# Performance work log

Measured on AMD Instinct MI355X. Metric: run time of the kernel, lower is better.

## Reference

```python
import jax, jax.numpy as jnp
import numpy as np


def _binop(ei, ej):
    # diagonal linear recurrence combine: (a_i, b_i) * (a_j, b_j) -> (a_j*a_i, a_j*b_i + b_j)
    ai, bi = ei
    aj, bj = ej
    return aj * ai, aj * bi + bj


def setup_inputs() -> dict:
    key = jax.random.key(0)
    ks = jax.random.split(key, 9)
    B_, T, D_in, D_out, N = 16, 2048, 512, 512, 512
    inp = {
        "input": jax.random.normal(ks[0], (B_, T, D_in), dtype=jnp.float32),
        "D": jax.random.normal(ks[1], (D_out, D_in), dtype=jnp.float32) / np.sqrt(D_in),
        "nu_log": jax.random.normal(ks[2], (N,), dtype=jnp.float32),
        "theta_log": jax.random.normal(ks[3], (N,), dtype=jnp.float32),
        "gamma_log": jax.random.normal(ks[4], (N,), dtype=jnp.float32),
        "B_re": jax.random.normal(ks[5], (N, D_in), dtype=jnp.float32) / np.sqrt(2 * D_in),
        "B_im": jax.random.normal(ks[6], (N, D_in), dtype=jnp.float32) / np.sqrt(2 * D_in),
        "C_re": jax.random.normal(ks[7], (D_out, N), dtype=jnp.float32) / np.sqrt(N),
        "C_im": jax.random.normal(ks[8], (D_out, N), dtype=jnp.float32) / np.sqrt(N),
    }
    return inp


def reference(input, D, nu_log, theta_log, gamma_log, B_re, B_im, C_re, C_im):
    # ss_params
    lam_abs = jnp.exp(-jnp.exp(nu_log))                      # [N]
    lam_phase = jnp.exp(theta_log)                           # [N]
    lam = lam_abs * (jnp.cos(lam_phase) + 1j * jnp.sin(lam_phase))  # complex [N]
    gamma = jnp.exp(gamma_log)                               # [N]
    Bc = (B_re + 1j * B_im) * gamma[:, None]                 # [N, D_in]
    Cc = C_re + 1j * C_im                                    # [D_out, N]

    # input projection: Bu_elements [batch, T, N] (complex)
    Bu = input.astype(Bc.dtype) @ Bc.T
    lam_el = jnp.broadcast_to(lam, Bu.shape)

    # parallel associative scan over time axis (initial state is zero)
    _, states = jax.lax.associative_scan(_binop, (lam_el, Bu), axis=1)

    # readout
    y = jnp.real(states @ Cc.T) + input @ D.T                # [batch, T, D_out]
    return y
```

## Files before the change

kernel.cpp:

```cpp
#include <hip/hip_runtime.h>
#include <hip/hip_fp16.h>

typedef _Float16 f16;
typedef __attribute__((ext_vector_type(8))) _Float16 f16x8;
typedef __attribute__((ext_vector_type(2))) _Float16 f16x2;
typedef __attribute__((ext_vector_type(4))) float f32x4;

#define B_SZ 16
#define T_SZ 2048
#define DIN 512
#define DOUT 512
#define N_SZ 512
#define M_SZ (B_SZ * T_SZ)
#define NCHUNK 16
#define LCHUNK 128

__device__ __forceinline__ void gload_lds16(const void* g, void* l) {
  __builtin_amdgcn_global_load_lds(
      (const __attribute__((address_space(1))) void*)g,
      (__attribute__((address_space(3))) void*)l, 16, 0, 0);
}


__global__ void prep_params(const float* __restrict__ nu_log,
                            const float* __restrict__ theta_log,
                            float2* __restrict__ lam2,
                            float2* __restrict__ lamL2) {
  int n = threadIdx.x;
  if (n < N_SZ) {
    float nu = expf(nu_log[n]);
    float ph = expf(theta_log[n]);
    float la = expf(-nu);
    lam2[n] = make_float2(la * cosf(ph), la * sinf(ph));
    float laL = expf(-nu * (float)LCHUNK);
    float phL = ph * (float)LCHUNK;
    lamL2[n] = make_float2(laL * cosf(phL), laL * sinf(phL));
  }
}

__global__ void prep_w1(const float* __restrict__ B_re, const float* __restrict__ B_im,
                        const float* __restrict__ gamma_log, f16* __restrict__ W1) {
  int tid = blockIdx.x * 256 + threadIdx.x;
  int np = tid >> 9;
  int d = tid & 511;
  int n = np >> 1;
  float g = expf(gamma_log[n]);
  const float* src = (np & 1) ? B_im : B_re;
  W1[(size_t)np * 512 + d] = (f16)(src[(size_t)n * 512 + d] * g);
}

__global__ void prep_w2(const float* __restrict__ C_re, const float* __restrict__ C_im,
                        const float* __restrict__ Dm, f16* __restrict__ W2) {
  int k = blockIdx.x * 256 + threadIdx.x;
  int j = blockIdx.y;
  float v;
  if (k < 512)       v =  C_re[(size_t)j * 512 + k];
  else if (k < 1024) v = -C_im[(size_t)j * 512 + (k - 512)];
  else               v =  Dm[(size_t)j * 512 + (k - 1024)];
  W2[(size_t)j * 1536 + k] = (f16)v;
}

__global__ void conv_input(const float* __restrict__ in, f16* __restrict__ A2) {
  int tid = blockIdx.x * 256 + threadIdx.x;
  int m = tid >> 6;
  int d0 = (tid & 63) << 3;
  const float4* p = (const float4*)(in + (size_t)m * DIN + d0);
  float4 a = p[0], b = p[1];
  f16x8 h;
  h[0] = (f16)a.x; h[1] = (f16)a.y; h[2] = (f16)a.z; h[3] = (f16)a.w;
  h[4] = (f16)b.x; h[5] = (f16)b.y; h[6] = (f16)b.z; h[7] = (f16)b.w;
  *(f16x8*)(A2 + (size_t)m * 1536 + 1024 + d0) = h;
}


__global__ void scan_a(const f16* __restrict__ Bu, const float2* __restrict__ lam2,
                       float2* __restrict__ S) {
  int tid = blockIdx.x * 256 + threadIdx.x;
  int n = tid & 511;
  int c = (tid >> 9) & (NCHUNK - 1);
  int b = tid >> 13;
  float2 l = lam2[n];
  const unsigned* bu = (const unsigned*)Bu + (size_t)(b * T_SZ + c * LCHUNK) * 512 + n;
  float sre = 0.f, sim = 0.f;
#pragma unroll 8
  for (int t = 0; t < LCHUNK; ++t) {
    unsigned u = bu[(size_t)t * 512];
    f16x2 h = __builtin_bit_cast(f16x2, u);
    float nre = l.x * sre - l.y * sim + (float)h.x;
    sim = l.x * sim + l.y * sre + (float)h.y;
    sre = nre;
  }
  S[(size_t)(b * NCHUNK + c) * 512 + n] = make_float2(sre, sim);
}

__global__ void scan_b(const float2* __restrict__ S, const float2* __restrict__ lamL2,
                       float2* __restrict__ Carry) {
  int tid = blockIdx.x * 256 + threadIdx.x;
  int n = tid & 511;
  int b = tid >> 9;
  float2 lL = lamL2[n];
  float cre = 0.f, cim = 0.f;
  for (int c = 0; c < NCHUNK; ++c) {
    size_t idx = (size_t)(b * NCHUNK + c) * 512 + n;
    Carry[idx] = make_float2(cre, cim);
    float2 s = S[idx];
    float nre = lL.x * cre - lL.y * cim + s.x;
    cim = lL.x * cim + lL.y * cre + s.y;
    cre = nre;
  }
}

__global__ void scan_c(const f16* __restrict__ Bu, const float2* __restrict__ lam2,
                       const float2* __restrict__ Carry, f16* __restrict__ A2) {
  int tid = blockIdx.x * 256 + threadIdx.x;
  int n = tid & 511;
  int c = (tid >> 9) & (NCHUNK - 1);
  int b = tid >> 13;
  float2 l = lam2[n];
  float2 car = Carry[(size_t)(b * NCHUNK + c) * 512 + n];
  float sre = car.x, sim = car.y;
  int m0 = b * T_SZ + c * LCHUNK;
  const unsigned* bu = (const unsigned*)Bu + (size_t)m0 * 512 + n;
  f16* outre = A2 + (size_t)m0 * 1536 + n;
#pragma unroll 4
  for (int t = 0; t < LCHUNK; ++t) {
    unsigned u = bu[(size_t)t * 512];
    f16x2 h = __builtin_bit_cast(f16x2, u);
    float nre = l.x * sre - l.y * sim + (float)h.x;
    sim = l.x * sim + l.y * sre + (float)h.y;
    sre = nre;
    outre[(size_t)t * 1536] = (f16)sre;
    outre[(size_t)t * 1536 + 512] = (f16)sim;
  }
}


template <typename CT>
__global__ __launch_bounds__(512, 2) void gemm256(
    const f16* __restrict__ A, int lda,
    const f16* __restrict__ Bm, int ldb,
    CT* __restrict__ C, int ldc, int K, int nxt) {
  extern __shared__ f16 smem[];
  f16* sA = smem;
  f16* sB = smem + 2 * 16384;

  const int tid = threadIdx.x;
  const int lane = tid & 63;
  const int wid = tid >> 6;
  const int wr = wid >> 2;
  const int wc = wid & 3;
  const int fr = lane & 15;
  const int fg = lane >> 4;
  const int xr = fr & 7;

  const int nwg = gridDim.x;
  const int id = blockIdx.x;
  const int swz = (id & 7) * (nwg >> 3) + (id >> 3);
  const int m0 = (swz / nxt) * 256;
  const int n0 = (swz % nxt) * 256;

  const int srow = tid >> 3;
  const int scol = ((tid & 7) ^ (srow & 7)) * 8;
  const int sdst = wid * 512;

  const int NT = K >> 6;

  f32x4 acc[8][4];
#pragma unroll
  for (int i = 0; i < 8; ++i)
#pragma unroll
    for (int j = 0; j < 4; ++j) acc[i][j] = f32x4{0.f, 0.f, 0.f, 0.f};

  auto stage = [&](int t) {
    const int b = t & 1;
    f16* dA = sA + b * 16384 + sdst;
    f16* dB = sB + b * 16384 + sdst;
    const f16* gA = A + (size_t)(m0 + srow) * lda + t * 64 + scol;
    const f16* gB = Bm + (size_t)(n0 + srow) * ldb + t * 64 + scol;
    gload_lds16(gA, dA);
    gload_lds16(gA + (size_t)64 * lda, dA + 4096);
    gload_lds16(gA + (size_t)128 * lda, dA + 8192);
    gload_lds16(gA + (size_t)192 * lda, dA + 12288);
    gload_lds16(gB, dB);
    gload_lds16(gB + (size_t)64 * ldb, dB + 4096);
    gload_lds16(gB + (size_t)128 * ldb, dB + 8192);
    gload_lds16(gB + (size_t)192 * ldb, dB + 12288);
  };

  auto barrier = [&]() {
    __builtin_amdgcn_sched_barrier(0);
    __builtin_amdgcn_s_barrier();
    __builtin_amdgcn_sched_barrier(0);
  };

  stage(0);
  asm volatile("s_waitcnt vmcnt(0)" ::: "memory");
  barrier();

  f16x8 bf[4][2];
  for (int t = 0; t < NT; ++t) {
    const int b = t & 1;
    const f16* bA = sA + b * 16384;
    const f16* bB = sB + b * 16384;
    if (t + 1 < NT) stage(t + 1);
#pragma unroll
    for (int h = 0; h < 4; ++h) {
      if (h == 0) {
#pragma unroll
        for (int nrep = 0; nrep < 4; ++nrep)
#pragma unroll
          for (int ks = 0; ks < 2; ++ks) {
            int row = wc * 64 + nrep * 16 + fr;
            bf[nrep][ks] =
                *(const f16x8*)(bB + row * 64 + (((ks * 4 + fg) ^ xr) * 8));
          }
      }
      f16x8 af[2][2];
#pragma unroll
      for (int mi = 0; mi < 2; ++mi)
#pragma unroll
        for (int ks = 0; ks < 2; ++ks) {
          int row = wr * 128 + (h * 2 + mi) * 16 + fr;
          af[mi][ks] =
              *(const f16x8*)(bA + row * 64 + (((ks * 4 + fg) ^ xr) * 8));
        }
      __builtin_amdgcn_s_setprio(1);
#pragma unroll
      for (int mi = 0; mi < 2; ++mi)
#pragma unroll
        for (int nrep = 0; nrep < 4; ++nrep)
#pragma unroll
          for (int ks = 0; ks < 2; ++ks)
            acc[h * 2 + mi][nrep] = __builtin_amdgcn_mfma_f32_16x16x32_f16(
                af[mi][ks], bf[nrep][ks], acc[h * 2 + mi][nrep], 0, 0, 0);
      __builtin_amdgcn_s_setprio(0);
      if (h == 3 && t + 1 < NT)
        asm volatile("s_waitcnt vmcnt(0)" ::: "memory");
      barrier();
    }
  }

#pragma unroll
  for (int mi = 0; mi < 8; ++mi) {
    int rbase = m0 + wr * 128 + mi * 16 + fg * 4;
#pragma unroll
    for (int ni = 0; ni < 4; ++ni) {
      int col = n0 + wc * 64 + ni * 16 + fr;
#pragma unroll
      for (int r = 0; r < 4; ++r)
        C[(size_t)(rbase + r) * ldc + col] = (CT)acc[mi][ni][r];
    }
  }
}


extern "C" void kernel_launch(void* const* d_in, const int* in_sizes, int n_in,
                              void* d_out, int out_size, void* d_ws, size_t ws_size,
                              hipStream_t stream) {
  const float* input = (const float*)d_in[0];
  const float* Dmat = (const float*)d_in[1];
  const float* nu_log = (const float*)d_in[2];
  const float* theta_log = (const float*)d_in[3];
  const float* gamma_log = (const float*)d_in[4];
  const float* B_re = (const float*)d_in[5];
  const float* B_im = (const float*)d_in[6];
  const float* C_re = (const float*)d_in[7];
  const float* C_im = (const float*)d_in[8];
  float* y = (float*)d_out;

  char* ws = (char*)d_ws;
  size_t off = 0;
  auto alloc = [&](size_t bytes) {
    void* p = ws + off;
    off = (off + bytes + 255) & ~(size_t)255;
    return p;
  };
  float2* lam2 = (float2*)alloc(N_SZ * sizeof(float2));
  float2* lamL2 = (float2*)alloc(N_SZ * sizeof(float2));
  f16* W1 = (f16*)alloc((size_t)2 * N_SZ * DIN * 2);
  f16* W2 = (f16*)alloc((size_t)DOUT * 1536 * 2);
  f16* A2 = (f16*)alloc((size_t)M_SZ * 1536 * 2);
  f16* Bu = (f16*)alloc((size_t)M_SZ * 2 * N_SZ * 2);
  float2* S = (float2*)alloc((size_t)B_SZ * NCHUNK * N_SZ * sizeof(float2));
  float2* Carry = (float2*)alloc((size_t)B_SZ * NCHUNK * N_SZ * sizeof(float2));

  const int shmem = 131072;
  {
    auto* g16 = gemm256<f16>;
    auto* g32 = gemm256<float>;
    hipFuncSetAttribute((const void*)g16,
                        hipFuncAttributeMaxDynamicSharedMemorySize, shmem);
    hipFuncSetAttribute((const void*)g32,
                        hipFuncAttributeMaxDynamicSharedMemorySize, shmem);
  }

  prep_params<<<1, 512, 0, stream>>>(nu_log, theta_log, lam2, lamL2);
  prep_w1<<<2048, 256, 0, stream>>>(B_re, B_im, gamma_log, W1);
  prep_w2<<<dim3(6, 512), 256, 0, stream>>>(C_re, C_im, Dmat, W2);
  conv_input<<<(M_SZ * DIN / 8) / 256, 256, 0, stream>>>(input, A2);

  gemm256<f16><<<512, 512, shmem, stream>>>(A2 + 1024, 1536, W1, 512, Bu, 1024, 512, 4);

  scan_a<<<(B_SZ * NCHUNK * N_SZ) / 256, 256, 0, stream>>>(Bu, lam2, S);
  scan_b<<<(B_SZ * N_SZ) / 256, 256, 0, stream>>>(S, lamL2, Carry);
  scan_c<<<(B_SZ * NCHUNK * N_SZ) / 256, 256, 0, stream>>>(Bu, lam2, Carry, A2);

  gemm256<float><<<256, 512, shmem, stream>>>(A2, 1536, W2, 1536, y, 512, 1536, 2);
}
```

Before: 169.1 us.

## Switch GEMM to 32x32x16 MFMA and fuse prep kernels into one launch

Replaces the 16x16x32 MFMA tiling in the GEMM with 32x32x16 MFMA instructions, cutting LDS fragment reads per flop and simplifying the K loop to one barrier per tile. The setprio hints and sub-phase interleaving are dropped. Merges the four parameter and input-conversion kernels into a single launch to reduce launch overhead. Risk: less overlap between LDS reads and MFMA within a tile.

```diff
diff --git a/kernel.cpp b/kernel.cpp
--- a/kernel.cpp
+++ b/kernel.cpp
@@ -4,7 +4,7 @@
 typedef _Float16 f16;
 typedef __attribute__((ext_vector_type(8))) _Float16 f16x8;
 typedef __attribute__((ext_vector_type(2))) _Float16 f16x2;
-typedef __attribute__((ext_vector_type(4))) float f32x4;
+typedef __attribute__((ext_vector_type(16))) float f32x16;
 
 #define B_SZ 16
 #define T_SZ 2048
@@ -22,12 +22,18 @@
 }
 
 
-__global__ void prep_params(const float* __restrict__ nu_log,
-                            const float* __restrict__ theta_log,
-                            float2* __restrict__ lam2,
-                            float2* __restrict__ lamL2) {
-  int n = threadIdx.x;
-  if (n < N_SZ) {
+__global__ void prep_all(const float* __restrict__ nu_log,
+                         const float* __restrict__ theta_log,
+                         const float* __restrict__ gamma_log,
+                         const float* __restrict__ B_re, const float* __restrict__ B_im,
+                         const float* __restrict__ C_re, const float* __restrict__ C_im,
+                         const float* __restrict__ Dm, const float* __restrict__ input,
+                         float2* __restrict__ lam2, float2* __restrict__ lamL2,
+                         f16* __restrict__ W1, f16* __restrict__ W2,
+                         f16* __restrict__ A2) {
+  int b = blockIdx.x;
+  if (b < 2) {
+    int n = b * 256 + threadIdx.x;
     float nu = expf(nu_log[n]);
     float ph = expf(theta_log[n]);
     float la = expf(-nu);
@@ -35,41 +41,34 @@
     float laL = expf(-nu * (float)LCHUNK);
     float phL = ph * (float)LCHUNK;
     lamL2[n] = make_float2(laL * cosf(phL), laL * sinf(phL));
-  }
-}
-
-__global__ void prep_w1(const float* __restrict__ B_re, const float* __restrict__ B_im,
-                        const float* __restrict__ gamma_log, f16* __restrict__ W1) {
-  int tid = blockIdx.x * 256 + threadIdx.x;
-  int np = tid >> 9;
-  int d = tid & 511;
-  int n = np >> 1;
-  float g = expf(gamma_log[n]);
-  const float* src = (np & 1) ? B_im : B_re;
-  W1[(size_t)np * 512 + d] = (f16)(src[(size_t)n * 512 + d] * g);
-}
-
-__global__ void prep_w2(const float* __restrict__ C_re, const float* __restrict__ C_im,
-                        const float* __restrict__ Dm, f16* __restrict__ W2) {
-  int k = blockIdx.x * 256 + threadIdx.x;
-  int j = blockIdx.y;
-  float v;
-  if (k < 512)       v =  C_re[(size_t)j * 512 + k];
-  else if (k < 1024) v = -C_im[(size_t)j * 512 + (k - 512)];
-  else               v =  Dm[(size_t)j * 512 + (k - 1024)];
-  W2[(size_t)j * 1536 + k] = (f16)v;
-}
-
-__global__ void conv_input(const float* __restrict__ in, f16* __restrict__ A2) {
-  int tid = blockIdx.x * 256 + threadIdx.x;
-  int m = tid >> 6;
-  int d0 = (tid & 63) << 3;
-  const float4* p = (const float4*)(in + (size_t)m * DIN + d0);
-  float4 a = p[0], b = p[1];
-  f16x8 h;
-  h[0] = (f16)a.x; h[1] = (f16)a.y; h[2] = (f16)a.z; h[3] = (f16)a.w;
-  h[4] = (f16)b.x; h[5] = (f16)b.y; h[6] = (f16)b.z; h[7] = (f16)b.w;
-  *(f16x8*)(A2 + (size_t)m * 1536 + 1024 + d0) = h;
+  } else if (b < 2 + 2048) {
+    int tid = (b - 2) * 256 + threadIdx.x;
+    int np = tid >> 9;
+    int d = tid & 511;
+    int n = np >> 1;
+    float g = expf(gamma_log[n]);
+    const float* src = (np & 1) ? B_im : B_re;
+    W1[(size_t)np * 512 + d] = (f16)(src[(size_t)n * 512 + d] * g);
+  } else if (b < 2 + 2048 + 3072) {
+    int tid = (b - 2050) * 256 + threadIdx.x;
+    int j = tid / 1536;
+    int k = tid - j * 1536;
+    float v;
+    if (k < 512)       v =  C_re[(size_t)j * 512 + k];
+    else if (k < 1024) v = -C_im[(size_t)j * 512 + (k - 512)];
+    else               v =  Dm[(size_t)j * 512 + (k - 1024)];
+    W2[(size_t)j * 1536 + k] = (f16)v;
+  } else {
+    int tid = (b - 5122) * 256 + threadIdx.x;
+    int m = tid >> 6;
+    int d0 = (tid & 63) << 3;
+    const float4* p = (const float4*)(input + (size_t)m * DIN + d0);
+    float4 a = p[0], c = p[1];
+    f16x8 h;
+    h[0] = (f16)a.x; h[1] = (f16)a.y; h[2] = (f16)a.z; h[3] = (f16)a.w;
+    h[4] = (f16)c.x; h[5] = (f16)c.y; h[6] = (f16)c.z; h[7] = (f16)c.w;
+    *(f16x8*)(A2 + (size_t)m * 1536 + 1024 + d0) = h;
+  }
 }
 
 
@@ -141,17 +140,14 @@
     const f16* __restrict__ Bm, int ldb,
     CT* __restrict__ C, int ldc, int K, int nxt) {
   extern __shared__ f16 smem[];
-  f16* sA = smem;
-  f16* sB = smem + 2 * 16384;
-
   const int tid = threadIdx.x;
   const int lane = tid & 63;
   const int wid = tid >> 6;
   const int wr = wid >> 2;
   const int wc = wid & 3;
-  const int fr = lane & 15;
-  const int fg = lane >> 4;
-  const int xr = fr & 7;
+  const int r32 = lane & 31;
+  const int khalf = lane >> 5;
+  const int key = r32 & 7;
 
   const int nwg = gridDim.x;
   const int id = blockIdx.x;
@@ -161,96 +157,71 @@
 
   const int srow = tid >> 3;
   const int scol = ((tid & 7) ^ (srow & 7)) * 8;
-  const int sdst = wid * 512;
-
   const int NT = K >> 6;
 
-  f32x4 acc[8][4];
-#pragma unroll
-  for (int i = 0; i < 8; ++i)
-#pragma unroll
-    for (int j = 0; j < 4; ++j) acc[i][j] = f32x4{0.f, 0.f, 0.f, 0.f};
+  f32x16 acc[4][2];
+#pragma unroll
+  for (int i = 0; i < 4; ++i)
+#pragma unroll
+    for (int j = 0; j < 2; ++j)
+#pragma unroll
+      for (int r = 0; r < 16; ++r) acc[i][j][r] = 0.f;
 
   auto stage = [&](int t) {
-    const int b = t & 1;
-    f16* dA = sA + b * 16384 + sdst;
-    f16* dB = sB + b * 16384 + sdst;
+    f16* base = smem + (t & 1) * 32768;
+    f16* dst = base + tid * 8;
     const f16* gA = A + (size_t)(m0 + srow) * lda + t * 64 + scol;
     const f16* gB = Bm + (size_t)(n0 + srow) * ldb + t * 64 + scol;
-    gload_lds16(gA, dA);
-    gload_lds16(gA + (size_t)64 * lda, dA + 4096);
-    gload_lds16(gA + (size_t)128 * lda, dA + 8192);
-    gload_lds16(gA + (size_t)192 * lda, dA + 12288);
-    gload_lds16(gB, dB);
-    gload_lds16(gB + (size_t)64 * ldb, dB + 4096);
-    gload_lds16(gB + (size_t)128 * ldb, dB + 8192);
-    gload_lds16(gB + (size_t)192 * ldb, dB + 12288);
+#pragma unroll
+    for (int i = 0; i < 4; ++i) {
+      gload_lds16(gA + (size_t)(i * 64) * lda, dst + i * 4096);
+      gload_lds16(gB + (size_t)(i * 64) * ldb, dst + 16384 + i * 4096);
+    }
   };
 
-  auto barrier = [&]() {
+  stage(0);
+  asm volatile("s_waitcnt vmcnt(0)" ::: "memory");
+  __builtin_amdgcn_sched_barrier(0);
+  __builtin_amdgcn_s_barrier();
+  __builtin_amdgcn_sched_barrier(0);
+
+  for (int t = 0; t < NT; ++t) {
+    if (t + 1 < NT) stage(t + 1);
+    const f16* bA = smem + (t & 1) * 32768;
+    const f16* bB = bA + 16384;
+#pragma unroll
+    for (int ks = 0; ks < 4; ++ks) {
+      const int so = ((ks * 2 + khalf) ^ key) * 8;
+      f16x8 af[4], bf[2];
+#pragma unroll
+      for (int mi = 0; mi < 4; ++mi)
+        af[mi] = *(const f16x8*)(bA + (wr * 128 + mi * 32 + r32) * 64 + so);
+#pragma unroll
+      for (int ni = 0; ni < 2; ++ni)
+        bf[ni] = *(const f16x8*)(bB + (wc * 64 + ni * 32 + r32) * 64 + so);
+#pragma unroll
+      for (int mi = 0; mi < 4; ++mi)
+#pragma unroll
+        for (int ni = 0; ni < 2; ++ni)
+          acc[mi][ni] = __builtin_amdgcn_mfma_f32_32x32x16_f16(
+              af[mi], bf[ni], acc[mi][ni], 0, 0, 0);
+    }
+    asm volatile("s_waitcnt vmcnt(0)" ::: "memory");
     __builtin_amdgcn_sched_barrier(0);
     __builtin_amdgcn_s_barrier();
     __builtin_amdgcn_sched_barrier(0);
-  };
-
-  stage(0);
-  asm volatile("s_waitcnt vmcnt(0)" ::: "memory");
-  barrier();
-
-  f16x8 bf[4][2];
-  for (int t = 0; t < NT; ++t) {
-    const int b = t & 1;
-    const f16* bA = sA + b * 16384;
-    const f16* bB = sB + b * 16384;
-    if (t + 1 < NT) stage(t + 1);
-#pragma unroll
-    for (int h = 0; h < 4; ++h) {
-      if (h == 0) {
-#pragma unroll
-        for (int nrep = 0; nrep < 4; ++nrep)
-#pragma unroll
-          for (int ks = 0; ks < 2; ++ks) {
-            int row = wc * 64 + nrep * 16 + fr;
-            bf[nrep][ks] =
-                *(const f16x8*)(bB + row * 64 + (((ks * 4 + fg) ^ xr) * 8));
-          }
+  }
+
+#pragma unroll
+  for (int mi = 0; mi < 4; ++mi)
+#pragma unroll
+    for (int ni = 0; ni < 2; ++ni)
+#pragma unroll
+      for (int r = 0; r < 16; ++r) {
+        int row = m0 + wr * 128 + mi * 32 + (r & 3) + ((r >> 2) * 8) + khalf * 4;
+        int col = n0 + wc * 64 + ni * 32 + r32;
+        C[(size_t)row * ldc + col] = (CT)acc[mi][ni][r];
       }
-      f16x8 af[2][2];
-#pragma unroll
-      for (int mi = 0; mi < 2; ++mi)
-#pragma unroll
-        for (int ks = 0; ks < 2; ++ks) {
-          int row = wr * 128 + (h * 2 + mi) * 16 + fr;
-          af[mi][ks] =
-              *(const f16x8*)(bA + row * 64 + (((ks * 4 + fg) ^ xr) * 8));
-        }
-      __builtin_amdgcn_s_setprio(1);
-#pragma unroll
-      for (int mi = 0; mi < 2; ++mi)
-#pragma unroll
-        for (int nrep = 0; nrep < 4; ++nrep)
-#pragma unroll
-          for (int ks = 0; ks < 2; ++ks)
-            acc[h * 2 + mi][nrep] = __builtin_amdgcn_mfma_f32_16x16x32_f16(
-                af[mi][ks], bf[nrep][ks], acc[h * 2 + mi][nrep], 0, 0, 0);
-      __builtin_amdgcn_s_setprio(0);
-      if (h == 3 && t + 1 < NT)
-        asm volatile("s_waitcnt vmcnt(0)" ::: "memory");
-      barrier();
-    }
-  }
-
-#pragma unroll
-  for (int mi = 0; mi < 8; ++mi) {
-    int rbase = m0 + wr * 128 + mi * 16 + fg * 4;
-#pragma unroll
-    for (int ni = 0; ni < 4; ++ni) {
-      int col = n0 + wc * 64 + ni * 16 + fr;
-#pragma unroll
-      for (int r = 0; r < 4; ++r)
-        C[(size_t)(rbase + r) * ldc + col] = (CT)acc[mi][ni][r];
-    }
-  }
 }
 
 
@@ -294,10 +265,8 @@
                         hipFuncAttributeMaxDynamicSharedMemorySize, shmem);
   }
 
-  prep_params<<<1, 512, 0, stream>>>(nu_log, theta_log, lam2, lamL2);
-  prep_w1<<<2048, 256, 0, stream>>>(B_re, B_im, gamma_log, W1);
-  prep_w2<<<dim3(6, 512), 256, 0, stream>>>(C_re, C_im, Dmat, W2);
-  conv_input<<<(M_SZ * DIN / 8) / 256, 256, 0, stream>>>(input, A2);
+  prep_all<<<13314, 256, 0, stream>>>(nu_log, theta_log, gamma_log, B_re, B_im,
+                                      C_re, C_im, Dmat, input, lam2, lamL2, W1, W2, A2);
 
   gemm256<f16><<<512, 512, shmem, stream>>>(A2 + 1024, 1536, W1, 512, Bu, 1024, 512, 4);
 
```

Result: faster. 164.5 us (-2.7%).

## Fuse local chunk scan into projection GEMM epilogue and apply carries in parallel

Applied to the files above, without the earlier changes.

The first GEMM now stages its accumulator tile in LDS and runs the intra-chunk recurrence over 64 timesteps directly in its epilogue. It writes the local scan states and the chunk-end sums, which removes the separate scan_a pass that re-read Bu. The sequential scan_c is replaced by a fully parallel apply_carry kernel that adds lambda^j times the carry using a precomputed power table. Chunk length drops to 64, and the four prep kernels are merged into one launch. The trade-off is a serial 64-step epilogue inside the GEMM and an extra intermediate buffer that is still written and read.

```diff
diff --git a/kernel.cpp b/kernel.cpp
--- a/kernel.cpp
+++ b/kernel.cpp
@@ -3,6 +3,7 @@
 
 typedef _Float16 f16;
 typedef __attribute__((ext_vector_type(8))) _Float16 f16x8;
+typedef __attribute__((ext_vector_type(4))) _Float16 f16x4;
 typedef __attribute__((ext_vector_type(2))) _Float16 f16x2;
 typedef __attribute__((ext_vector_type(4))) float f32x4;
 
@@ -12,8 +13,8 @@
 #define DOUT 512
 #define N_SZ 512
 #define M_SZ (B_SZ * T_SZ)
-#define NCHUNK 16
-#define LCHUNK 128
+#define LCHUNK 64
+#define NCHUNK 32
 
 __device__ __forceinline__ void gload_lds16(const void* g, void* l) {
   __builtin_amdgcn_global_load_lds(
@@ -22,12 +23,19 @@
 }
 
 
-__global__ void prep_params(const float* __restrict__ nu_log,
-                            const float* __restrict__ theta_log,
-                            float2* __restrict__ lam2,
-                            float2* __restrict__ lamL2) {
-  int n = threadIdx.x;
-  if (n < N_SZ) {
+__global__ void prep_all(const float* __restrict__ nu_log,
+                         const float* __restrict__ theta_log,
+                         const float* __restrict__ gamma_log,
+                         const float* __restrict__ B_re, const float* __restrict__ B_im,
+                         const float* __restrict__ C_re, const float* __restrict__ C_im,
+                         const float* __restrict__ Dm, const float* __restrict__ input,
+                         float2* __restrict__ lam2, float2* __restrict__ lamL2,
+                         float2* __restrict__ lamp,
+                         f16* __restrict__ W1, f16* __restrict__ W2,
+                         f16* __restrict__ A2) {
+  int b = blockIdx.x;
+  if (b < 2) {
+    int n = b * 256 + threadIdx.x;
     float nu = expf(nu_log[n]);
     float ph = expf(theta_log[n]);
     float la = expf(-nu);
@@ -35,63 +43,49 @@
     float laL = expf(-nu * (float)LCHUNK);
     float phL = ph * (float)LCHUNK;
     lamL2[n] = make_float2(laL * cosf(phL), laL * sinf(phL));
-  }
-}
-
-__global__ void prep_w1(const float* __restrict__ B_re, const float* __restrict__ B_im,
-                        const float* __restrict__ gamma_log, f16* __restrict__ W1) {
-  int tid = blockIdx.x * 256 + threadIdx.x;
-  int np = tid >> 9;
-  int d = tid & 511;
-  int n = np >> 1;
-  float g = expf(gamma_log[n]);
-  const float* src = (np & 1) ? B_im : B_re;
-  W1[(size_t)np * 512 + d] = (f16)(src[(size_t)n * 512 + d] * g);
-}
-
-__global__ void prep_w2(const float* __restrict__ C_re, const float* __restrict__ C_im,
-                        const float* __restrict__ Dm, f16* __restrict__ W2) {
-  int k = blockIdx.x * 256 + threadIdx.x;
-  int j = blockIdx.y;
-  float v;
-  if (k < 512)       v =  C_re[(size_t)j * 512 + k];
-  else if (k < 1024) v = -C_im[(size_t)j * 512 + (k - 512)];
-  else               v =  Dm[(size_t)j * 512 + (k - 1024)];
-  W2[(size_t)j * 1536 + k] = (f16)v;
-}
-
-__global__ void conv_input(const float* __restrict__ in, f16* __restrict__ A2) {
-  int tid = blockIdx.x * 256 + threadIdx.x;
-  int m = tid >> 6;
-  int d0 = (tid & 63) << 3;
-  const float4* p = (const float4*)(in + (size_t)m * DIN + d0);
-  float4 a = p[0], b = p[1];
-  f16x8 h;
-  h[0] = (f16)a.x; h[1] = (f16)a.y; h[2] = (f16)a.z; h[3] = (f16)a.w;
-  h[4] = (f16)b.x; h[5] = (f16)b.y; h[6] = (f16)b.z; h[7] = (f16)b.w;
-  *(f16x8*)(A2 + (size_t)m * 1536 + 1024 + d0) = h;
-}
-
-
-__global__ void scan_a(const f16* __restrict__ Bu, const float2* __restrict__ lam2,
-                       float2* __restrict__ S) {
-  int tid = blockIdx.x * 256 + threadIdx.x;
-  int n = tid & 511;
-  int c = (tid >> 9) & (NCHUNK - 1);
-  int b = tid >> 13;
-  float2 l = lam2[n];
-  const unsigned* bu = (const unsigned*)Bu + (size_t)(b * T_SZ + c * LCHUNK) * 512 + n;
-  float sre = 0.f, sim = 0.f;
-#pragma unroll 8
-  for (int t = 0; t < LCHUNK; ++t) {
-    unsigned u = bu[(size_t)t * 512];
-    f16x2 h = __builtin_bit_cast(f16x2, u);
-    float nre = l.x * sre - l.y * sim + (float)h.x;
-    sim = l.x * sim + l.y * sre + (float)h.y;
-    sre = nre;
-  }
-  S[(size_t)(b * NCHUNK + c) * 512 + n] = make_float2(sre, sim);
-}
+  } else if (b < 4) {
+    int n = (b - 2) * 256 + threadIdx.x;
+    float nu = expf(nu_log[n]);
+    float ph = expf(theta_log[n]);
+    float la = expf(-nu);
+    float2 l1 = make_float2(la * cosf(ph), la * sinf(ph));
+    float2 cur = l1;
+    for (int j = 0; j < LCHUNK; ++j) {
+      lamp[(size_t)j * 512 + n] = cur;
+      float nre = cur.x * l1.x - cur.y * l1.y;
+      cur.y = cur.x * l1.y + cur.y * l1.x;
+      cur.x = nre;
+    }
+  } else if (b < 4 + 2048) {
+    int tid = (b - 4) * 256 + threadIdx.x;
+    int np = tid >> 9;
+    int d = tid & 511;
+    int n = np >> 1;
+    float g = expf(gamma_log[n]);
+    const float* src = (np & 1) ? B_im : B_re;
+    W1[(size_t)np * 512 + d] = (f16)(src[(size_t)n * 512 + d] * g);
+  } else if (b < 4 + 2048 + 3072) {
+    int tid = (b - 2052) * 256 + threadIdx.x;
+    int j = tid / 1536;
+    int k = tid - j * 1536;
+    float v;
+    if (k < 512)       v =  C_re[(size_t)j * 512 + k];
+    else if (k < 1024) v = -C_im[(size_t)j * 512 + (k - 512)];
+    else               v =  Dm[(size_t)j * 512 + (k - 1024)];
+    W2[(size_t)j * 1536 + k] = (f16)v;
+  } else {
+    int tid = (b - 5124) * 256 + threadIdx.x;
+    int m = tid >> 6;
+    int d0 = (tid & 63) << 3;
+    const float4* p = (const float4*)(input + (size_t)m * DIN + d0);
+    float4 a = p[0], c = p[1];
+    f16x8 h;
+    h[0] = (f16)a.x; h[1] = (f16)a.y; h[2] = (f16)a.z; h[3] = (f16)a.w;
+    h[4] = (f16)c.x; h[5] = (f16)c.y; h[6] = (f16)c.z; h[7] = (f16)c.w;
+    *(f16x8*)(A2 + (size_t)m * 1536 + 1024 + d0) = h;
+  }
+}
+
 
 __global__ void scan_b(const float2* __restrict__ S, const float2* __restrict__ lamL2,
                        float2* __restrict__ Carry) {
@@ -110,36 +104,41 @@
   }
 }
 
-__global__ void scan_c(const f16* __restrict__ Bu, const float2* __restrict__ lam2,
-                       const float2* __restrict__ Carry, f16* __restrict__ A2) {
+__global__ void apply_carry(const unsigned* __restrict__ sloc,
+                            const float2* __restrict__ lamp,
+                            const float2* __restrict__ Carry,
+                            f16* __restrict__ A2) {
   int tid = blockIdx.x * 256 + threadIdx.x;
-  int n = tid & 511;
-  int c = (tid >> 9) & (NCHUNK - 1);
-  int b = tid >> 13;
-  float2 l = lam2[n];
-  float2 car = Carry[(size_t)(b * NCHUNK + c) * 512 + n];
-  float sre = car.x, sim = car.y;
-  int m0 = b * T_SZ + c * LCHUNK;
-  const unsigned* bu = (const unsigned*)Bu + (size_t)m0 * 512 + n;
-  f16* outre = A2 + (size_t)m0 * 1536 + n;
-#pragma unroll 4
-  for (int t = 0; t < LCHUNK; ++t) {
-    unsigned u = bu[(size_t)t * 512];
-    f16x2 h = __builtin_bit_cast(f16x2, u);
-    float nre = l.x * sre - l.y * sim + (float)h.x;
-    sim = l.x * sim + l.y * sre + (float)h.y;
-    sre = nre;
-    outre[(size_t)t * 1536] = (f16)sre;
-    outre[(size_t)t * 1536 + 512] = (f16)sim;
-  }
-}
-
-
-template <typename CT>
+  int g = tid & 127;
+  int m = tid >> 7;
+  int j = m & 63;
+  int bc = m >> 6;
+  int n0 = g * 4;
+  const float2* lpp = lamp + (size_t)j * 512 + n0;
+  const float2* crp = Carry + (size_t)bc * 512 + n0;
+  uint4 sv = *(const uint4*)(sloc + (size_t)m * 512 + n0);
+  unsigned u4[4] = {sv.x, sv.y, sv.z, sv.w};
+  f16x4 ore, oim;
+#pragma unroll
+  for (int q = 0; q < 4; ++q) {
+    f16x2 u = __builtin_bit_cast(f16x2, u4[q]);
+    float2 lp = lpp[q];
+    float2 cr = crp[q];
+    ore[q] = (f16)((float)u.x + lp.x * cr.x - lp.y * cr.y);
+    oim[q] = (f16)((float)u.y + lp.x * cr.y + lp.y * cr.x);
+  }
+  *(f16x4*)(A2 + (size_t)m * 1536 + n0) = ore;
+  *(f16x4*)(A2 + (size_t)m * 1536 + 512 + n0) = oim;
+}
+
+
+template <typename CT, bool FUSE>
 __global__ __launch_bounds__(512, 2) void gemm256(
     const f16* __restrict__ A, int lda,
     const f16* __restrict__ Bm, int ldb,
-    CT* __restrict__ C, int ldc, int K, int nxt) {
+    CT* __restrict__ C, int ldc, int K, int nxt,
+    const float2* __restrict__ lam2, unsigned* __restrict__ sloc,
+    float2* __restrict__ Svec) {
   extern __shared__ f16 smem[];
   f16* sA = smem;
   f16* sB = smem + 2 * 16384;
@@ -170,6 +169,9 @@
   for (int i = 0; i < 8; ++i)
 #pragma unroll
     for (int j = 0; j < 4; ++j) acc[i][j] = f32x4{0.f, 0.f, 0.f, 0.f};
+
+  const int ar0 = wr * 128;
+  const int bc0 = wc * 64;
 
   auto stage = [&](int t) {
     const int b = t & 1;
@@ -210,7 +212,7 @@
         for (int nrep = 0; nrep < 4; ++nrep)
 #pragma unroll
           for (int ks = 0; ks < 2; ++ks) {
-            int row = wc * 64 + nrep * 16 + fr;
+            int row = bc0 + nrep * 16 + fr;
             bf[nrep][ks] =
                 *(const f16x8*)(bB + row * 64 + (((ks * 4 + fg) ^ xr) * 8));
           }
@@ -220,7 +222,7 @@
       for (int mi = 0; mi < 2; ++mi)
 #pragma unroll
         for (int ks = 0; ks < 2; ++ks) {
-          int row = wr * 128 + (h * 2 + mi) * 16 + fr;
+          int row = ar0 + (h * 2 + mi) * 16 + fr;
           af[mi][ks] =
               *(const f16x8*)(bA + row * 64 + (((ks * 4 + fg) ^ xr) * 8));
         }
@@ -240,15 +242,53 @@
     }
   }
 
-#pragma unroll
-  for (int mi = 0; mi < 8; ++mi) {
-    int rbase = m0 + wr * 128 + mi * 16 + fg * 4;
-#pragma unroll
-    for (int ni = 0; ni < 4; ++ni) {
-      int col = n0 + wc * 64 + ni * 16 + fr;
-#pragma unroll
-      for (int r = 0; r < 4; ++r)
-        C[(size_t)(rbase + r) * ldc + col] = (CT)acc[mi][ni][r];
+  if constexpr (FUSE) {
+    f16* reg = smem + wid * 8192;
+#pragma unroll
+    for (int mi = 0; mi < 8; ++mi)
+#pragma unroll
+      for (int ni = 0; ni < 4; ++ni)
+#pragma unroll
+        for (int r = 0; r < 4; ++r)
+          reg[(mi * 16 + fg * 4 + r) * 64 + ni * 16 + fr] = (f16)acc[mi][ni][r];
+    __syncthreads();
+    const int half = lane >> 5;
+    const int nc = lane & 31;
+    const int n = ((n0 + wc * 64) >> 1) + nc;
+    const float2 l2 = lam2[n];
+    const f16* col = smem + wid * 8192 + (half * 64) * 64 + 2 * nc;
+    const int mbase = m0 + wr * 128 + half * 64;
+    unsigned* sp = sloc + (size_t)mbase * 512 + n;
+    float sre = 0.f, sim = 0.f;
+#pragma unroll 1
+    for (int j0 = 0; j0 < 64; j0 += 8) {
+      f16x2 u[8];
+#pragma unroll
+      for (int q = 0; q < 8; ++q) u[q] = *(const f16x2*)(col + (j0 + q) * 64);
+#pragma unroll
+      for (int q = 0; q < 8; ++q) {
+        float nre = l2.x * sre - l2.y * sim + (float)u[q].x;
+        sim = l2.x * sim + l2.y * sre + (float)u[q].y;
+        sre = nre;
+        f16x2 o;
+        o.x = (f16)sre;
+        o.y = (f16)sim;
+        sp[(size_t)(j0 + q) * 512] = __builtin_bit_cast(unsigned, o);
+      }
+    }
+    Svec[(size_t)((m0 >> 11) * NCHUNK + ((mbase >> 6) & (NCHUNK - 1))) * 512 + n] =
+        make_float2(sre, sim);
+  } else {
+#pragma unroll
+    for (int mi = 0; mi < 8; ++mi) {
+      int rbase = m0 + ar0 + mi * 16 + fg * 4;
+#pragma unroll
+      for (int ni = 0; ni < 4; ++ni) {
+        int col = n0 + bc0 + ni * 16 + fr;
+#pragma unroll
+        for (int r = 0; r < 4; ++r)
+          C[(size_t)(rbase + r) * ldc + col] = (CT)acc[mi][ni][r];
+      }
     }
   }
 }
@@ -277,33 +317,35 @@
   };
   float2* lam2 = (float2*)alloc(N_SZ * sizeof(float2));
   float2* lamL2 = (float2*)alloc(N_SZ * sizeof(float2));
+  float2* lamp = (float2*)alloc((size_t)LCHUNK * N_SZ * sizeof(float2));
   f16* W1 = (f16*)alloc((size_t)2 * N_SZ * DIN * 2);
   f16* W2 = (f16*)alloc((size_t)DOUT * 1536 * 2);
   f16* A2 = (f16*)alloc((size_t)M_SZ * 1536 * 2);
-  f16* Bu = (f16*)alloc((size_t)M_SZ * 2 * N_SZ * 2);
+  unsigned* sloc = (unsigned*)alloc((size_t)M_SZ * N_SZ * 4);
   float2* S = (float2*)alloc((size_t)B_SZ * NCHUNK * N_SZ * sizeof(float2));
   float2* Carry = (float2*)alloc((size_t)B_SZ * NCHUNK * N_SZ * sizeof(float2));
 
   const int shmem = 131072;
   {
-    auto* g16 = gemm256<f16>;
-    auto* g32 = gemm256<float>;
-    hipFuncSetAttribute((const void*)g16,
+    auto* g1 = gemm256<f16, true>;
+    auto* g2 = gemm256<float, false>;
+    hipFuncSetAttribute((const void*)g1,
                         hipFuncAttributeMaxDynamicSharedMemorySize, shmem);
-    hipFuncSetAttribute((const void*)g32,
+    hipFuncSetAttribute((const void*)g2,
                         hipFuncAttributeMaxDynamicSharedMemorySize, shmem);
   }
 
-  prep_params<<<1, 512, 0, stream>>>(nu_log, theta_log, lam2, lamL2);
-  prep_w1<<<2048, 256, 0, stream>>>(B_re, B_im, gamma_log, W1);
-  prep_w2<<<dim3(6, 512), 256, 0, stream>>>(C_re, C_im, Dmat, W2);
-  conv_input<<<(M_SZ * DIN / 8) / 256, 256, 0, stream>>>(input, A2);
-
-  gemm256<f16><<<512, 512, shmem, stream>>>(A2 + 1024, 1536, W1, 512, Bu, 1024, 512, 4);
-
-  scan_a<<<(B_SZ * NCHUNK * N_SZ) / 256, 256, 0, stream>>>(Bu, lam2, S);
+  prep_all<<<13316, 256, 0, stream>>>(nu_log, theta_log, gamma_log, B_re, B_im,
+                                      C_re, C_im, Dmat, input, lam2, lamL2, lamp,
+                                      W1, W2, A2);
+
+  gemm256<f16, true><<<512, 512, shmem, stream>>>(
+      A2 + 1024, 1536, W1, 512, (f16*)nullptr, 0, 512, 4, lam2, sloc, S);
+
   scan_b<<<(B_SZ * N_SZ) / 256, 256, 0, stream>>>(S, lamL2, Carry);
-  scan_c<<<(B_SZ * NCHUNK * N_SZ) / 256, 256, 0, stream>>>(Bu, lam2, Carry, A2);
-
-  gemm256<float><<<256, 512, shmem, stream>>>(A2, 1536, W2, 1536, y, 512, 1536, 2);
-}
+
+  apply_carry<<<(M_SZ * 128) / 256, 256, 0, stream>>>(sloc, lamp, Carry, A2);
+
+  gemm256<float, false><<<256, 512, shmem, stream>>>(
+      A2, 1536, W2, 1536, y, 512, 1536, 2, nullptr, nullptr, nullptr);
+}
```

Measured after the change: 154.3 us. -8.8%, faster.
